# Kernel optimization log

Measured on AMD Instinct MI355X. Metric: run time of the kernel, lower is better.

Reference implementation:

```python
import jax, jax.numpy as jnp
import numpy as np

D = 768       # model dim (mha.input_dim)
M = 16        # memory tokens
S = 1024      # input sequence length
B = 16        # batch
SCALE = 1.0 / np.sqrt(D).astype(np.float32)  # mha.scaling


def setup_inputs() -> dict:
    key = jax.random.key(0)
    ks = jax.random.split(key, 11)
    x = jax.random.normal(ks[0], (B, S, D), dtype=jnp.float32)
    mask = jnp.zeros((S, S + M), dtype=jnp.float32)  # additive mask over [q_len, kv_len]
    memory = jax.random.normal(ks[1], (1, M, D), dtype=jnp.float32) * 0.02
    wq = jax.random.normal(ks[2], (D, D), dtype=jnp.float32) / np.sqrt(D)
    bq = jnp.zeros((D,), dtype=jnp.float32)
    wk = jax.random.normal(ks[3], (D, D), dtype=jnp.float32) / np.sqrt(D)
    bk = jnp.zeros((D,), dtype=jnp.float32)
    wv = jax.random.normal(ks[4], (D, D), dtype=jnp.float32) / np.sqrt(D)
    bv = jnp.zeros((D,), dtype=jnp.float32)
    wo = jax.random.normal(ks[5], (D, D), dtype=jnp.float32) / np.sqrt(D)
    bo = jnp.zeros((D,), dtype=jnp.float32)
    return {"x": x, "mask": mask, "memory": memory,
            "wq": wq, "bq": bq, "wk": wk, "bk": bk,
            "wv": wv, "bv": bv, "wo": wo, "bo": bo}


def reference(x, mask, memory, wq, bq, wk, bk, wv, bv, wo, bo):
    # concat learnable memory tokens onto the key/value stream
    mem = jnp.broadcast_to(memory, (x.shape[0], M, D))
    kv_in = jnp.concatenate([x, mem], axis=1)            # [B, S+M, D]
    q = jnp.einsum('bsd,ed->bse', x, wq) + bq            # [B, S,   D]
    k = jnp.einsum('btd,ed->bte', kv_in, wk) + bk        # [B, S+M, D]
    v = jnp.einsum('btd,ed->bte', kv_in, wv) + bv        # [B, S+M, D]
    scores = jnp.einsum('bse,bte->bst', q, k) * SCALE    # [B, S, S+M]
    attn = jax.nn.softmax(scores + mask, axis=-1)
    head_out = jnp.einsum('bst,bte->bse', attn, v)       # [B, S, D]
    attended = jnp.einsum('bse,fe->bsf', head_out, wo) + bo
    return attended[:, :S, :]                            # split(...)[0]: first S tokens
```

## Files before the change

kernel.cpp:

```cpp
#include <hip/hip_runtime.h>
#include <math.h>
#include <stdint.h>

#define D_    768
#define B_    16
#define S_    1024
#define M_    16
#define SM_   1040
#define SMP_  1088
#define SCALE_ 0.036084392f

typedef __bf16 bf16;
typedef __attribute__((ext_vector_type(8))) __bf16 bf16x8;
typedef __attribute__((ext_vector_type(4))) __bf16 bf16x4;
typedef __attribute__((ext_vector_type(4))) float  f32x4;

#define GL16(gp, lp) __builtin_amdgcn_global_load_lds( \
    (const __attribute__((address_space(1))) void*)(gp), \
    (__attribute__((address_space(3))) void*)(lp), 16, 0, 0)

template<int OUTMODE, int GM>
__launch_bounds__(256, 3)
__global__ void gemm_k(const bf16*  __restrict__ Am,
                       const bf16*  __restrict__ Bm,
                       const float* __restrict__ aux,
                       void* __restrict__ Cout,
                       void* __restrict__ C2,
                       void* __restrict__ C3,
                       int lda, int ldb, int ldc,
                       int K, int colsB,
                       long sA, long sB, long sC)
{
    __shared__ __attribute__((aligned(16))) bf16 As[128 * 64];
    __shared__ __attribute__((aligned(16))) bf16 Bs[128 * 64];

    const int t    = threadIdx.x;
    const int l    = t & 63;
    const int wv   = t >> 6;

    int row0, col0, z;
    if (GM == 1) {
        const int bid = blockIdx.x;
        const int xcd = bid & 7, s = bid >> 3;
        z = xcd * 2 + s / 72;
        const int r = s % 72;
        row0 = (r & 7) * 128; col0 = (r >> 3) * 128;
    } else if (GM == 2) {
        const int bid = blockIdx.x;
        const int xcd = bid & 7, s = bid >> 3;
        z = xcd * 2 + s / 48;
        const int r = s % 48;
        row0 = (r & 7) * 128; col0 = (r >> 3) * 128;
    } else {
        const int gx  = gridDim.x;
        const int nwg = gx * gridDim.y;
        const int bid = blockIdx.y * gx + blockIdx.x;
        const int qn  = nwg >> 3, rr = nwg & 7;
        const int xcd = bid & 7,  idx = bid >> 3;
        const int wg  = (xcd < rr ? xcd * (qn + 1)
                                  : rr * (qn + 1) + (xcd - rr) * qn) + idx;
        row0 = (wg / gx) * 128; col0 = (wg % gx) * 128; z = 0;
    }

    const bf16* agb[4];
    const bf16* bgb[4];
    #pragma unroll
    for (int i = 0; i < 4; ++i) {
        const int r = (wv * 4 + i) * 8 + (l >> 3);
        const int c = (l & 7) ^ (r & 7);
        agb[i] = Am + (size_t)z * sA + (size_t)(row0 + r) * lda + c * 8;
        int bcol = col0 + r;
        if (bcol > colsB - 1) bcol = colsB - 1;
        bgb[i] = Bm + (size_t)z * sB + (size_t)bcol * ldb + c * 8;
    }

    f32x4 acc[4][4];
    #pragma unroll
    for (int i = 0; i < 4; ++i)
        #pragma unroll
        for (int j = 0; j < 4; ++j)
            acc[i][j] = (f32x4){0.f, 0.f, 0.f, 0.f};

    const int wr0 = (wv & 1) * 64;
    const int wc0 = (wv >> 1) * 64;
    const int lq  = l >> 4;
    const int lm  = l & 15;

    for (int kt = 0; kt < K; kt += 64) {
        __syncthreads();
        #pragma unroll
        for (int i = 0; i < 4; ++i)
            GL16(agb[i] + kt, &As[(wv * 4 + i) * 512]);
        #pragma unroll
        for (int i = 0; i < 4; ++i)
            GL16(bgb[i] + kt, &Bs[(wv * 4 + i) * 512]);
        __syncthreads();

        #pragma unroll
        for (int ks = 0; ks < 2; ++ks) {
            bf16x8 af[4], bfr[4];
            #pragma unroll
            for (int i = 0; i < 4; ++i) {
                const int rowA = wr0 + i * 16 + lm;
                const int p = (ks * 4 + lq) ^ (rowA & 7);
                af[i] = *(const bf16x8*)&As[rowA * 64 + p * 8];
            }
            #pragma unroll
            for (int j = 0; j < 4; ++j) {
                const int rowB = wc0 + j * 16 + lm;
                const int p = (ks * 4 + lq) ^ (rowB & 7);
                bfr[j] = *(const bf16x8*)&Bs[rowB * 64 + p * 8];
            }
            #pragma unroll
            for (int i = 0; i < 4; ++i)
                #pragma unroll
                for (int j = 0; j < 4; ++j)
                    acc[i][j] = __builtin_amdgcn_mfma_f32_16x16x32_bf16(
                        af[i], bfr[j], acc[i][j], 0, 0, 0);
        }
    }

    if (OUTMODE == 4) {
        const bf16* em = (const bf16*)C3;
        float* rsum = (float*)C2;
        #pragma unroll
        for (int i = 0; i < 4; ++i) {
            const int t0 = row0 + wr0 + i * 16 + lq * 4;
            #pragma unroll
            for (int r = 0; r < 4; ++r) {
                float part = 0.f;
                #pragma unroll
                for (int j = 0; j < 4; ++j) {
                    const int gcol = col0 + wc0 + j * 16 + lm;
                    float val = 0.f;
                    if (gcol < SM_)
                        val = __expf(acc[i][j][r])
                            * (float)em[(size_t)(t0 + r) * SM_ + gcol];
                    const bf16 vb = (bf16)val;
                    part += (float)vb;
                    if (gcol < SMP_)
                        ((bf16*)Cout)[(size_t)z * sC
                            + (size_t)(t0 + r) * ldc + gcol] = vb;
                }
                #pragma unroll
                for (int o = 8; o; o >>= 1) part += __shfl_xor(part, o);
                if (lm == 0)
                    atomicAdd(&rsum[z * S_ + t0 + r], part);
            }
        }
        return;
    }

    float rin[4][4];
    if (OUTMODE == 5) {
        #pragma unroll
        for (int i = 0; i < 4; ++i) {
            const int t0 = row0 + wr0 + i * 16 + lq * 4;
            #pragma unroll
            for (int r = 0; r < 4; ++r)
                rin[i][r] = 1.f / aux[z * S_ + t0 + r];
        }
    }

    const int wsel = (OUTMODE == 3) ? (col0 / 768) : 0;
    #pragma unroll
    for (int j = 0; j < 4; ++j) {
        const int gcol = col0 + wc0 + j * 16 + lm;
        #pragma unroll
        for (int i = 0; i < 4; ++i) {
            const int t0 = row0 + wr0 + i * 16 + lq * 4;
            if (OUTMODE == 3) {
                const int lcol = gcol - wsel * 768;
                const float bv = aux[gcol];
                const int b  = t0 / SM_;
                const int tt = t0 - b * SM_;
                if (wsel == 0) {
                    if (tt < S_) {
                        #pragma unroll
                        for (int r = 0; r < 4; ++r)
                            ((bf16*)Cout)[((size_t)b * S_ + tt + r) * D_ + lcol]
                                = (bf16)(acc[i][j][r] + bv);
                    }
                } else if (wsel == 1) {
                    #pragma unroll
                    for (int r = 0; r < 4; ++r)
                        ((bf16*)C2)[(size_t)(t0 + r) * D_ + lcol]
                            = (bf16)(acc[i][j][r] + bv);
                } else {
                    bf16x4 o;
                    #pragma unroll
                    for (int r = 0; r < 4; ++r) o[r] = (bf16)(acc[i][j][r] + bv);
                    *(bf16x4*)((bf16*)C3 +
                        ((size_t)b * D_ + lcol) * SMP_ + tt) = o;
                }
            } else if (OUTMODE == 5) {
                #pragma unroll
                for (int r = 0; r < 4; ++r)
                    ((bf16*)Cout)[(size_t)z * sC + (size_t)(t0 + r) * ldc + gcol]
                        = (bf16)(acc[i][j][r] * rin[i][r]);
            } else {
                if (gcol < colsB) {
                    const float bv = aux ? aux[gcol] : 0.f;
                    #pragma unroll
                    for (int r = 0; r < 4; ++r)
                        ((float*)Cout)[(size_t)z * sC
                            + (size_t)(t0 + r) * ldc + gcol]
                            = acc[i][j][r] + bv;
                }
            }
        }
    }
}

__global__ void castw4_k(const float* __restrict__ w0, const float* __restrict__ w1,
                         const float* __restrict__ w2, const float* __restrict__ w3,
                         bf16* __restrict__ wqkv, bf16* __restrict__ wob)
{
    const float* in;
    bf16* out;
    float sc = 1.f;
    const size_t NW = (size_t)D_ * D_;
    switch (blockIdx.y) {
        case 0: in = w0; out = wqkv;          sc = SCALE_; break;
        case 1: in = w1; out = wqkv + NW;     break;
        case 2: in = w2; out = wqkv + 2 * NW; break;
        default: in = w3; out = wob;          break;
    }
    const int i = blockIdx.x * blockDim.x + threadIdx.x;
    const float4 f = ((const float4*)in)[i];
    bf16x4 v;
    v[0] = (bf16)(f.x * sc); v[1] = (bf16)(f.y * sc);
    v[2] = (bf16)(f.z * sc); v[3] = (bf16)(f.w * sc);
    ((bf16x4*)out)[i] = v;
}

__global__ void emask_k(const float* __restrict__ mask, bf16* __restrict__ em)
{
    const int i = blockIdx.x * blockDim.x + threadIdx.x;
    const float4 f = ((const float4*)mask)[i];
    bf16x4 v;
    v[0] = (bf16)__expf(f.x); v[1] = (bf16)__expf(f.y);
    v[2] = (bf16)__expf(f.z); v[3] = (bf16)__expf(f.w);
    ((bf16x4*)em)[i] = v;
}

__global__ void castx_k(const float* __restrict__ x, const float* __restrict__ mem,
                        bf16* __restrict__ cs,
                        const float* __restrict__ bq, const float* __restrict__ bk,
                        const float* __restrict__ bv, float* __restrict__ bqkv,
                        float* __restrict__ rsum)
{
    if (blockIdx.x == 6240) {
        const int tid = threadIdx.x;
        if (tid < 576) {
            const int g = tid * 4;
            float4 f;
            if (g < 768) {
                f = *(const float4*)(bq + g);
                f.x *= SCALE_; f.y *= SCALE_; f.z *= SCALE_; f.w *= SCALE_;
            } else if (g < 1536) {
                f = *(const float4*)(bk + g - 768);
            } else {
                f = *(const float4*)(bv + g - 1536);
            }
            *(float4*)(bqkv + g) = f;
        }
        const float4 zz = make_float4(0.f, 0.f, 0.f, 0.f);
        #pragma unroll
        for (int k = 0; k < 16; ++k)
            *(float4*)(rsum + tid * 64 + k * 4) = zz;
        return;
    }
    const int i = blockIdx.x * blockDim.x + threadIdx.x;
    const int row = i / 96;
    const int c8  = (i - row * 96) * 8;
    const int b   = row / SM_;
    const int tt  = row - b * SM_;
    const float* src = (tt < S_) ? (x + ((size_t)b * S_ + tt) * D_ + c8)
                                 : (mem + (size_t)(tt - S_) * D_ + c8);
    const float4 f0 = *(const float4*)src;
    const float4 f1 = *(const float4*)(src + 4);
    bf16x8 v;
    v[0] = (bf16)f0.x; v[1] = (bf16)f0.y; v[2] = (bf16)f0.z; v[3] = (bf16)f0.w;
    v[4] = (bf16)f1.x; v[5] = (bf16)f1.y; v[6] = (bf16)f1.z; v[7] = (bf16)f1.w;
    *(bf16x8*)(cs + (size_t)row * D_ + c8) = v;
}

extern "C" void kernel_launch(void* const* d_in, const int* in_sizes, int n_in,
                              void* d_out, int out_size, void* d_ws, size_t ws_size,
                              hipStream_t stream) {
    const float* x    = (const float*)d_in[0];
    const float* mask = (const float*)d_in[1];
    const float* mem  = (const float*)d_in[2];
    const float* wq   = (const float*)d_in[3];
    const float* bq   = (const float*)d_in[4];
    const float* wk   = (const float*)d_in[5];
    const float* bk   = (const float*)d_in[6];
    const float* wv   = (const float*)d_in[7];
    const float* bv   = (const float*)d_in[8];
    const float* wo   = (const float*)d_in[9];
    const float* bo   = (const float*)d_in[10];

    bf16* w = (bf16*)d_ws;
    const size_t NW  = (size_t)D_ * D_;
    const size_t NCS = (size_t)B_ * SM_ * D_;
    const size_t NQ  = (size_t)B_ * S_ * D_;
    const size_t NKV = (size_t)B_ * SM_ * D_;
    const size_t NVT = (size_t)B_ * D_ * SMP_;
    const size_t NEM = (size_t)S_ * SM_;
    bf16* wqkv = w;
    bf16* wob  = wqkv + 3 * NW;
    bf16* emb  = wob + NW;
    bf16* cs   = emb + NEM;
    bf16* qb   = cs  + NCS;
    bf16* kb   = qb  + NQ;
    bf16* vtb  = kb  + NKV;
    bf16* Pb   = vtb + NVT;
    float* bqkv = (float*)(Pb + (size_t)B_ * S_ * SMP_);
    float* rsum = bqkv + 2304;

    castw4_k<<<dim3(576, 4), 256, 0, stream>>>(wq, wk, wv, wo, wqkv, wob);
    emask_k<<<1040, 256, 0, stream>>>(mask, emb);
    castx_k<<<6241, 256, 0, stream>>>(x, mem, cs, bq, bk, bv, bqkv, rsum);

    gemm_k<3, 3><<<dim3(18, 130), 256, 0, stream>>>(
        cs, wqkv, bqkv, qb, kb, vtb, D_, D_, 0, D_, 3 * D_, 0, 0, 0);

    gemm_k<4, 1><<<1152, 256, 0, stream>>>(
        qb, kb, nullptr, Pb, rsum, emb, D_, D_, SMP_, D_, SM_,
        (long)S_ * D_, (long)SM_ * D_, (long)S_ * SMP_);

    gemm_k<5, 2><<<768, 256, 0, stream>>>(
        Pb, vtb, rsum, cs, nullptr, nullptr, SMP_, SMP_, D_, SMP_, D_,
        (long)S_ * SMP_, (long)D_ * SMP_, (long)S_ * D_);

    gemm_k<1, 3><<<dim3(6, 128), 256, 0, stream>>>(
        cs, wob, bo, d_out, nullptr, nullptr, D_, D_, D_, D_, D_, 0, 0, 0);
}
```

Baseline: 338.0 us.

## Triple-buffer GEMM K-loop with async global-to-LDS prefetch and single barrier

```diff
diff --git a/kernel.cpp b/kernel.cpp
--- a/kernel.cpp
+++ b/kernel.cpp
@@ -31,8 +31,8 @@
                        int K, int colsB,
                        long sA, long sB, long sC)
 {
-    __shared__ __attribute__((aligned(16))) bf16 As[128 * 64];
-    __shared__ __attribute__((aligned(16))) bf16 Bs[128 * 64];
+    __shared__ __attribute__((aligned(16))) bf16 As[3 * 128 * 32];
+    __shared__ __attribute__((aligned(16))) bf16 Bs[3 * 128 * 32];
 
     const int t    = threadIdx.x;
     const int l    = t & 63;
@@ -62,17 +62,28 @@
         row0 = (wg / gx) * 128; col0 = (wg % gx) * 128; z = 0;
     }
 
-    const bf16* agb[4];
-    const bf16* bgb[4];
+    const int rSt = wv * 16 + (l >> 2);
+    const int cSt = l & 3;
+    const bf16* aSt[2];
+    const bf16* bSt[2];
     #pragma unroll
-    for (int i = 0; i < 4; ++i) {
-        const int r = (wv * 4 + i) * 8 + (l >> 3);
-        const int c = (l & 7) ^ (r & 7);
-        agb[i] = Am + (size_t)z * sA + (size_t)(row0 + r) * lda + c * 8;
-        int bcol = col0 + r;
-        if (bcol > colsB - 1) bcol = colsB - 1;
-        bgb[i] = Bm + (size_t)z * sB + (size_t)bcol * ldb + c * 8;
-    }
+    for (int q = 0; q < 2; ++q) {
+        const int rL = rSt + q * 64;
+        const int sc = cSt ^ ((rL >> 1) & 3);
+        aSt[q] = Am + (size_t)z * sA + (size_t)(row0 + rL) * lda + sc * 8;
+        int bc = col0 + rL;
+        if (bc > colsB - 1) bc = colsB - 1;
+        bSt[q] = Bm + (size_t)z * sB + (size_t)bc * ldb + sc * 8;
+    }
+
+    auto stage = [&](int buf, int kt) {
+        #pragma unroll
+        for (int q = 0; q < 2; ++q)
+            GL16(aSt[q] + kt, &As[buf * 4096 + q * 2048 + wv * 512]);
+        #pragma unroll
+        for (int q = 0; q < 2; ++q)
+            GL16(bSt[q] + kt, &Bs[buf * 4096 + q * 2048 + wv * 512]);
+    };
 
     f32x4 acc[4][4];
     #pragma unroll
@@ -86,38 +97,42 @@
     const int lq  = l >> 4;
     const int lm  = l & 15;
 
-    for (int kt = 0; kt < K; kt += 64) {
-        __syncthreads();
+    const int nT = K >> 5;
+    int br = 0, bw = 2;
+
+    stage(0, 0);
+    stage(1, 32);
+
+    for (int tt = 0; tt < nT; ++tt) {
+        if (tt < nT - 1) asm volatile("s_waitcnt vmcnt(4)" ::: "memory");
+        else             asm volatile("s_waitcnt vmcnt(0)" ::: "memory");
+        __builtin_amdgcn_s_barrier();
+
+        bf16x8 af[4], bfr[4];
+        #pragma unroll
+        for (int i = 0; i < 4; ++i) {
+            const int rowA = wr0 + i * 16 + lm;
+            const int p = lq ^ ((rowA >> 1) & 3);
+            af[i] = *(const bf16x8*)&As[br * 4096 + rowA * 32 + p * 8];
+        }
+        #pragma unroll
+        for (int j = 0; j < 4; ++j) {
+            const int rowB = wc0 + j * 16 + lm;
+            const int p = lq ^ ((rowB >> 1) & 3);
+            bfr[j] = *(const bf16x8*)&Bs[br * 4096 + rowB * 32 + p * 8];
+        }
+
+        if (tt + 2 < nT) stage(bw, (tt + 2) << 5);
+
         #pragma unroll
         for (int i = 0; i < 4; ++i)
-            GL16(agb[i] + kt, &As[(wv * 4 + i) * 512]);
-        #pragma unroll
-        for (int i = 0; i < 4; ++i)
-            GL16(bgb[i] + kt, &Bs[(wv * 4 + i) * 512]);
-        __syncthreads();
-
-        #pragma unroll
-        for (int ks = 0; ks < 2; ++ks) {
-            bf16x8 af[4], bfr[4];
             #pragma unroll
-            for (int i = 0; i < 4; ++i) {
-                const int rowA = wr0 + i * 16 + lm;
-                const int p = (ks * 4 + lq) ^ (rowA & 7);
-                af[i] = *(const bf16x8*)&As[rowA * 64 + p * 8];
-            }
-            #pragma unroll
-            for (int j = 0; j < 4; ++j) {
-                const int rowB = wc0 + j * 16 + lm;
-                const int p = (ks * 4 + lq) ^ (rowB & 7);
-                bfr[j] = *(const bf16x8*)&Bs[rowB * 64 + p * 8];
-            }
-            #pragma unroll
-            for (int i = 0; i < 4; ++i)
-                #pragma unroll
-                for (int j = 0; j < 4; ++j)
-                    acc[i][j] = __builtin_amdgcn_mfma_f32_16x16x32_bf16(
-                        af[i], bfr[j], acc[i][j], 0, 0, 0);
-        }
+            for (int j = 0; j < 4; ++j)
+                acc[i][j] = __builtin_amdgcn_mfma_f32_16x16x32_bf16(
+                    af[i], bfr[j], acc[i][j], 0, 0, 0);
+
+        br = (br == 2) ? 0 : br + 1;
+        bw = (bw == 2) ? 0 : bw + 1;
     }
 
     if (OUTMODE == 4) {
```

Measured after the change: 366.6 us. 8.5% more time.

## Stage GEMM epilogues through shared memory for coalesced vector stores

Applied to the files above, without the earlier changes.

```diff
diff --git a/kernel.cpp b/kernel.cpp
--- a/kernel.cpp
+++ b/kernel.cpp
@@ -31,8 +31,9 @@
                        int K, int colsB,
                        long sA, long sB, long sC)
 {
-    __shared__ __attribute__((aligned(16))) bf16 As[128 * 64];
-    __shared__ __attribute__((aligned(16))) bf16 Bs[128 * 64];
+    __shared__ __attribute__((aligned(16))) bf16 Ls[16384];
+    bf16* As = Ls;
+    bf16* Bs = Ls + 8192;
 
     const int t    = threadIdx.x;
     const int l    = t & 63;
@@ -120,93 +121,177 @@
         }
     }
 
+    __syncthreads();
+
     if (OUTMODE == 4) {
-        const bf16* em = (const bf16*)C3;
+        const int lr = l >> 4;
+        const int pc = l & 15;
+        #pragma unroll
+        for (int g = 0; g < 8; ++g) {
+            const int row = wv * 32 + g * 4 + lr;
+            const int sc  = pc ^ ((row & 7) << 1);
+            int gc = col0 + sc * 8;
+            if (gc > 1032) gc = 1032;
+            GL16((const bf16*)C3 + (size_t)(row0 + row) * SM_ + gc,
+                 &Ls[(wv * 32 + g * 4) * 128]);
+        }
+        asm volatile("s_waitcnt vmcnt(0)" ::: "memory");
+        __syncthreads();
         float* rsum = (float*)C2;
+        #pragma unroll
+        for (int i = 0; i < 4; ++i) {
+            #pragma unroll
+            for (int r = 0; r < 4; ++r) {
+                const int row = wr0 + i * 16 + lq * 4 + r;
+                float part = 0.f;
+                #pragma unroll
+                for (int j = 0; j < 4; ++j) {
+                    const int col  = wc0 + j * 16 + lm;
+                    const int gcol = col0 + col;
+                    const int idx  = row * 128
+                        + (((col >> 3) ^ ((row & 7) << 1)) * 8) + (col & 7);
+                    float val = 0.f;
+                    if (gcol < SM_)
+                        val = __expf(acc[i][j][r]) * (float)Ls[idx];
+                    const bf16 vb = (bf16)val;
+                    part += (float)vb;
+                    Ls[idx] = vb;
+                }
+                #pragma unroll
+                for (int o = 8; o; o >>= 1) part += __shfl_xor(part, o);
+                if (lm == 0)
+                    atomicAdd(&rsum[z * S_ + row0 + row], part);
+            }
+        }
+        __syncthreads();
+        #pragma unroll
+        for (int c = 0; c < 8; ++c) {
+            const int row = wv * 32 + c * 4 + lr;
+            bf16x8 v = *(const bf16x8*)&Ls[row * 128 + pc * 8];
+            const int gcol = col0 + (pc ^ ((row & 7) << 1)) * 8;
+            if (gcol < SMP_)
+                *(bf16x8*)((bf16*)Cout + (size_t)z * sC
+                           + (size_t)(row0 + row) * ldc + gcol) = v;
+        }
+        return;
+    }
+
+    bf16* W = Ls + wv * 4096;
+
+    if (OUTMODE == 5) {
+        float rin[4][4];
         #pragma unroll
         for (int i = 0; i < 4; ++i) {
             const int t0 = row0 + wr0 + i * 16 + lq * 4;
             #pragma unroll
-            for (int r = 0; r < 4; ++r) {
-                float part = 0.f;
-                #pragma unroll
-                for (int j = 0; j < 4; ++j) {
-                    const int gcol = col0 + wc0 + j * 16 + lm;
-                    float val = 0.f;
-                    if (gcol < SM_)
-                        val = __expf(acc[i][j][r])
-                            * (float)em[(size_t)(t0 + r) * SM_ + gcol];
-                    const bf16 vb = (bf16)val;
-                    part += (float)vb;
-                    if (gcol < SMP_)
-                        ((bf16*)Cout)[(size_t)z * sC
-                            + (size_t)(t0 + r) * ldc + gcol] = vb;
-                }
-                #pragma unroll
-                for (int o = 8; o; o >>= 1) part += __shfl_xor(part, o);
-                if (lm == 0)
-                    atomicAdd(&rsum[z * S_ + t0 + r], part);
-            }
-        }
-        return;
-    }
-
-    float rin[4][4];
-    if (OUTMODE == 5) {
-        #pragma unroll
-        for (int i = 0; i < 4; ++i) {
-            const int t0 = row0 + wr0 + i * 16 + lq * 4;
-            #pragma unroll
             for (int r = 0; r < 4; ++r)
                 rin[i][r] = 1.f / aux[z * S_ + t0 + r];
         }
-    }
-
-    const int wsel = (OUTMODE == 3) ? (col0 / 768) : 0;
+        #pragma unroll
+        for (int i = 0; i < 4; ++i)
+            #pragma unroll
+            for (int j = 0; j < 4; ++j)
+                #pragma unroll
+                for (int r = 0; r < 4; ++r) {
+                    const int row = i * 16 + lq * 4 + r;
+                    const int col = j * 16 + lm;
+                    W[row * 64 + (((col >> 3) ^ (row & 7)) * 8) + (col & 7)]
+                        = (bf16)(acc[i][j][r] * rin[i][r]);
+                }
+        __syncthreads();
+        #pragma unroll
+        for (int c = 0; c < 8; ++c) {
+            const int row = c * 8 + (l >> 3);
+            const int q8  = l & 7;
+            bf16x8 v = *(const bf16x8*)&W[row * 64 + q8 * 8];
+            const int gcol = col0 + wc0 + (q8 ^ (row & 7)) * 8;
+            const int grow = row0 + wr0 + row;
+            *(bf16x8*)((bf16*)Cout + (size_t)z * sC
+                       + (size_t)grow * ldc + gcol) = v;
+        }
+        return;
+    }
+
+    if (OUTMODE == 3) {
+        const int wsel = col0 / 768;
+        const int colb = col0 + wc0;
+        if (wsel < 2) {
+            #pragma unroll
+            for (int i = 0; i < 4; ++i)
+                #pragma unroll
+                for (int j = 0; j < 4; ++j) {
+                    const float bv = aux[colb + j * 16 + lm];
+                    #pragma unroll
+                    for (int r = 0; r < 4; ++r) {
+                        const int row = i * 16 + lq * 4 + r;
+                        const int col = j * 16 + lm;
+                        W[row * 64 + (((col >> 3) ^ (row & 7)) * 8) + (col & 7)]
+                            = (bf16)(acc[i][j][r] + bv);
+                    }
+                }
+            __syncthreads();
+            #pragma unroll
+            for (int c = 0; c < 8; ++c) {
+                const int row = c * 8 + (l >> 3);
+                const int q8  = l & 7;
+                bf16x8 v = *(const bf16x8*)&W[row * 64 + q8 * 8];
+                const int lcol = colb - wsel * 768 + (q8 ^ (row & 7)) * 8;
+                const int grow = row0 + wr0 + row;
+                if (wsel == 0) {
+                    const int b  = grow / SM_;
+                    const int tt = grow - b * SM_;
+                    if (tt < S_)
+                        *(bf16x8*)((bf16*)Cout
+                            + ((size_t)b * S_ + tt) * D_ + lcol) = v;
+                } else {
+                    *(bf16x8*)((bf16*)C2 + (size_t)grow * D_ + lcol) = v;
+                }
+            }
+        } else {
+            #pragma unroll
+            for (int i = 0; i < 4; ++i)
+                #pragma unroll
+                for (int j = 0; j < 4; ++j) {
+                    const float bv = aux[colb + j * 16 + lm];
+                    #pragma unroll
+                    for (int r = 0; r < 4; ++r) {
+                        const int trow = i * 16 + lq * 4 + r;
+                        const int e    = j * 16 + lm;
+                        W[e * 64 + (((trow >> 3) ^ (e & 7)) * 8) + (trow & 7)]
+                            = (bf16)(acc[i][j][r] + bv);
+                    }
+                }
+            __syncthreads();
+            #pragma unroll
+            for (int c = 0; c < 8; ++c) {
+                const int e  = c * 8 + (l >> 3);
+                const int q8 = l & 7;
+                bf16x8 v = *(const bf16x8*)&W[e * 64 + q8 * 8];
+                const int tl   = (q8 ^ (e & 7)) * 8;
+                const int grow = row0 + wr0 + tl;
+                const int b    = grow / SM_;
+                const int tt   = grow - b * SM_;
+                const int eg   = colb - 1536 + e;
+                *(bf16x8*)((bf16*)C3
+                    + ((size_t)b * D_ + eg) * SMP_ + tt) = v;
+            }
+        }
+        return;
+    }
+
     #pragma unroll
     for (int j = 0; j < 4; ++j) {
         const int gcol = col0 + wc0 + j * 16 + lm;
         #pragma unroll
         for (int i = 0; i < 4; ++i) {
             const int t0 = row0 + wr0 + i * 16 + lq * 4;
-            if (OUTMODE == 3) {
-                const int lcol = gcol - wsel * 768;
-                const float bv = aux[gcol];
-                const int b  = t0 / SM_;
-                const int tt = t0 - b * SM_;
-                if (wsel == 0) {
-                    if (tt < S_) {
-                        #pragma unroll
-                        for (int r = 0; r < 4; ++r)
-                            ((bf16*)Cout)[((size_t)b * S_ + tt + r) * D_ + lcol]
-                                = (bf16)(acc[i][j][r] + bv);
-                    }
-                } else if (wsel == 1) {
-                    #pragma unroll
-                    for (int r = 0; r < 4; ++r)
-                        ((bf16*)C2)[(size_t)(t0 + r) * D_ + lcol]
-                            = (bf16)(acc[i][j][r] + bv);
-                } else {
-                    bf16x4 o;
-                    #pragma unroll
-                    for (int r = 0; r < 4; ++r) o[r] = (bf16)(acc[i][j][r] + bv);
-                    *(bf16x4*)((bf16*)C3 +
-                        ((size_t)b * D_ + lcol) * SMP_ + tt) = o;
-                }
-            } else if (OUTMODE == 5) {
+            if (gcol < colsB) {
+                const float bv = aux ? aux[gcol] : 0.f;
                 #pragma unroll
                 for (int r = 0; r < 4; ++r)
-                    ((bf16*)Cout)[(size_t)z * sC + (size_t)(t0 + r) * ldc + gcol]
-                        = (bf16)(acc[i][j][r] * rin[i][r]);
-            } else {
-                if (gcol < colsB) {
-                    const float bv = aux ? aux[gcol] : 0.f;
-                    #pragma unroll
-                    for (int r = 0; r < 4; ++r)
-                        ((float*)Cout)[(size_t)z * sC
-                            + (size_t)(t0 + r) * ldc + gcol]
-                            = acc[i][j][r] + bv;
-                }
+                    ((float*)Cout)[(size_t)z * sC
+                        + (size_t)(t0 + r) * ldc + gcol]
+                        = acc[i][j][r] + bv;
             }
         }
     }
```

Result: faster. 315.4 us (-6.7%).
